# Kernel tuning notes

Hardware: AMD Instinct MI355X
Metric: run time of the kernel (lower is better)

## Reference

```python
import jax, jax.numpy as jnp
import numpy as np
import math

N_QUBITS = 6
N_LAYERS = 3
OUT_DIM = 8
B = 131072
F = 24


def _gate_rx(a):
    # RX(a) = [[cos(a/2), -i sin(a/2)], [-i sin(a/2), cos(a/2)]]; a: scalar or [B]
    c = jnp.cos(a / 2).astype(jnp.complex64)
    s = (-1j * jnp.sin(a / 2)).astype(jnp.complex64)
    return jnp.stack([jnp.stack([c, s], -1), jnp.stack([s, c], -1)], -2)


def _gate_ry(a):
    c = jnp.cos(a / 2).astype(jnp.complex64)
    s = jnp.sin(a / 2).astype(jnp.complex64)
    return jnp.stack([jnp.stack([c, -s], -1), jnp.stack([s, c], -1)], -2)


def _gate_rz(a):
    # RZ(a) = diag(e^{-ia/2}, e^{ia/2})
    e = jnp.exp(-0.5j * a.astype(jnp.complex64))
    z = jnp.zeros_like(e)
    return jnp.stack([jnp.stack([e, z], -1), jnp.stack([z, jnp.conj(e)], -1)], -2)


def _apply_1q(state, gate, q, batched):
    # state: [B] + [2]*N_QUBITS ; gate: [2,2] or [B,2,2]
    s = jnp.moveaxis(state, 1 + q, 1)
    if batched:
        out = jnp.einsum('bij,bj...->bi...', gate, s)
    else:
        out = jnp.einsum('ij,bj...->bi...', gate, s)
    return jnp.moveaxis(out, 1, 1 + q)


def _apply_cnot(state, c, t):
    # flip target where control bit == 1
    cax = 1 + c
    s0 = jnp.take(state, 0, axis=cax)
    s1 = jnp.take(state, 1, axis=cax)
    tax = 1 + t if t < c else t  # control axis removed
    s1 = jnp.flip(s1, axis=tax)
    return jnp.stack([s0, s1], axis=cax)


def _circuit(x, theta):
    Bn = x.shape[0]
    # pooling branch of forward: chunks of size ceil(F/n_qubits)=4, mean each
    x_packed = x.reshape(Bn, N_QUBITS, F // N_QUBITS).mean(-1)
    angles = jnp.clip(x_packed, -6.0, 6.0) / 6.0 * math.pi  # [B, n_qubits]

    state = jnp.zeros((Bn,) + (2,) * N_QUBITS, dtype=jnp.complex64)
    state = state.at[(slice(None),) + (0,) * N_QUBITS].set(1.0)

    # angle encoding: RX(a_q), RZ(0.5*a_q) per qubit (batched gates)
    for q in range(N_QUBITS):
        state = _apply_1q(state, _gate_rx(angles[:, q]), q, batched=True)
        state = _apply_1q(state, _gate_rz(0.5 * angles[:, q]), q, batched=True)

    for l in range(N_LAYERS):
        for q in range(N_QUBITS - 1):
            state = _apply_cnot(state, q, q + 1)
        state = _apply_cnot(state, N_QUBITS - 1, 0)
        for q in range(N_QUBITS):
            state = _apply_1q(state, _gate_rx(theta[l, q, 0]), q, batched=False)
            state = _apply_1q(state, _gate_ry(theta[l, q, 1]), q, batched=False)
            state = _apply_1q(state, _gate_rz(theta[l, q, 2]), q, batched=False)

    probs = jnp.abs(state) ** 2  # real
    meas = []
    for k in range(OUT_DIM):
        q = k % N_QUBITS
        if k % 2 == 0:  # PauliZ
            pq = jnp.sum(probs, axis=tuple(a for a in range(1, N_QUBITS + 1) if a != 1 + q))
            meas.append(pq[:, 0] - pq[:, 1])
        else:  # PauliX: Re <psi| X_q |psi>
            flipped = jnp.flip(state, axis=1 + q)
            meas.append(jnp.real(jnp.sum(jnp.conj(state) * flipped, axis=tuple(range(1, N_QUBITS + 1)))))
    return jnp.stack(meas, axis=1).astype(jnp.float32)  # [B, out_dim]


def setup_inputs() -> dict:
    key = jax.random.key(0)
    k1, k2 = jax.random.split(key)
    x = jax.random.normal(k1, (B, F), dtype=jnp.float32)
    theta = jax.random.normal(k2, (N_LAYERS, N_QUBITS, 3), dtype=jnp.float32) * 0.1
    return {"x": x, "theta": theta}


def reference(x, theta):
    return _circuit(x, theta)
```

## Files before the change

### kernel.cpp

```cpp
#include <hip/hip_runtime.h>
#include <math.h>


struct cf { float r, i; };

__device__ __forceinline__ cf cmul(cf a, cf b) {
    return { fmaf(a.r, b.r, -a.i * b.i), fmaf(a.r, b.i, a.i * b.r) };
}
__device__ __forceinline__ cf cmac(cf acc, cf g, cf v) {
    acc.r = fmaf(g.r, v.r, fmaf(-g.i, v.i, acc.r));
    acc.i = fmaf(g.r, v.i, fmaf(g.i, v.r, acc.i));
    return acc;
}

template<int M>
__device__ __forceinline__ void apply1q(cf* st, cf g00, cf g01, cf g10, cf g11) {
#pragma unroll
    for (int i = 0; i < 64; ++i) {
        if (i & M) continue;
        cf a = st[i], b = st[i + M];
        cf na = cmul(g00, a); na = cmac(na, g01, b);
        cf nb = cmul(g10, a); nb = cmac(nb, g11, b);
        st[i] = na; st[i + M] = nb;
    }
}

template<int MC, int MT>
__device__ __forceinline__ void cnot(cf* st) {
#pragma unroll
    for (int i = 0; i < 64; ++i) {
        if ((i & MC) && !(i & MT)) {
            cf tmp = st[i]; st[i] = st[i + MT]; st[i + MT] = tmp;
        }
    }
}

__global__ __launch_bounds__(256, 2) void qsim_kernel(
    const float* __restrict__ x, const float* __restrict__ theta,
    float* __restrict__ out) {
    __shared__ float gs[18 * 8];
    const int t = threadIdx.x;
    if (t < 18) {
        const float* th = theta + t * 3;
        float sx, cx, sy, cy, sz, cz;
        __sincosf(0.5f * th[0], &sx, &cx);
        __sincosf(0.5f * th[1], &sy, &cy);
        __sincosf(0.5f * th[2], &sz, &cz);
        cf m00 = {  cy * cx,  sy * sx };
        cf m01 = { -sy * cx, -cy * sx };
        cf m10 = {  sy * cx, -cy * sx };
        cf m11 = {  cy * cx, -sy * sx };
        cf e0 = { cz, -sz }, e1 = { cz, sz };
        cf g00 = cmul(e0, m00), g01 = cmul(e0, m01);
        cf g10 = cmul(e1, m10), g11 = cmul(e1, m11);
        float* o = gs + t * 8;
        o[0] = g00.r; o[1] = g00.i; o[2] = g01.r; o[3] = g01.i;
        o[4] = g10.r; o[5] = g10.i; o[6] = g11.r; o[7] = g11.i;
    }
    __syncthreads();

    const int b = blockIdx.x * 256 + t;

    const float4* xv = reinterpret_cast<const float4*>(x + (size_t)b * 24);
    cf v0[6], v1[6];
#pragma unroll
    for (int q = 0; q < 6; ++q) {
        float4 xq = xv[q];
        float m = (xq.x + xq.y + xq.z + xq.w) * 0.25f;
        m = fminf(fmaxf(m, -6.0f), 6.0f);
        float a = m * 0.52359877559829887308f;
        float s2, c2, s4, c4;
        __sincosf(0.50f * a, &s2, &c2);
        __sincosf(0.25f * a, &s4, &c4);
        v0[q] = { c4 * c2, -s4 * c2 };
        v1[q] = { s4 * s2, -c4 * s2 };
    }

    cf st[64];
    st[0] = v0[0]; st[32] = v1[0];
#pragma unroll
    for (int q = 1; q < 6; ++q) {
        const int m = 32 >> q;
#pragma unroll
        for (int i = 0; i < 64; i += 2 * m) {
            st[i + m] = cmul(st[i], v1[q]);
            st[i]     = cmul(st[i], v0[q]);
        }
    }

#pragma unroll
    for (int l = 0; l < 3; ++l) {
        cnot<32, 16>(st);
        cnot<16,  8>(st);
        cnot< 8,  4>(st);
        cnot< 4,  2>(st);
        cnot< 2,  1>(st);
        cnot< 1, 32>(st);
        const float* g = gs + l * 48;
#define G4(o) cf{g[(o)+0], g[(o)+1]}, cf{g[(o)+2], g[(o)+3]}, \
              cf{g[(o)+4], g[(o)+5]}, cf{g[(o)+6], g[(o)+7]}
        apply1q<32>(st, G4(0));
        apply1q<16>(st, G4(8));
        apply1q< 8>(st, G4(16));
        apply1q< 4>(st, G4(24));
        apply1q< 2>(st, G4(32));
        apply1q< 1>(st, G4(40));
#undef G4
    }

    float s[8] = {0, 0, 0, 0, 0, 0, 0, 0};
#pragma unroll
    for (int i = 0; i < 64; ++i) {
        float p = fmaf(st[i].r, st[i].r, st[i].i * st[i].i);
        const int gi = (((i >> 5) & 1) << 2) | (((i >> 3) & 1) << 1) | ((i >> 1) & 1);
        s[gi] += p;
    }
    float z0 = (s[0] + s[1] + s[2] + s[3]) - (s[4] + s[5] + s[6] + s[7]);
    float z2 = (s[0] + s[1] + s[4] + s[5]) - (s[2] + s[3] + s[6] + s[7]);
    float z4 = (s[0] + s[2] + s[4] + s[6]) - (s[1] + s[3] + s[5] + s[7]);

    float x1 = 0.0f, x3 = 0.0f, x5 = 0.0f;
#pragma unroll
    for (int i = 0; i < 64; ++i) {
        if (!(i & 16)) x1 = fmaf(st[i].r, st[i + 16].r, fmaf(st[i].i, st[i + 16].i, x1));
        if (!(i &  4)) x3 = fmaf(st[i].r, st[i +  4].r, fmaf(st[i].i, st[i +  4].i, x3));
        if (!(i &  1)) x5 = fmaf(st[i].r, st[i +  1].r, fmaf(st[i].i, st[i +  1].i, x5));
    }
    x1 *= 2.0f; x3 *= 2.0f; x5 *= 2.0f;

    float4* ov = reinterpret_cast<float4*>(out + (size_t)b * 8);
    ov[0] = make_float4(z0, x1, z2, x3);
    ov[1] = make_float4(z4, x5, z0, x1);
}

extern "C" void kernel_launch(void* const* d_in, const int* in_sizes, int n_in,
                              void* d_out, int out_size, void* d_ws, size_t ws_size,
                              hipStream_t stream) {
    const float* x     = (const float*)d_in[0];
    const float* theta = (const float*)d_in[1];
    float* out = (float*)d_out;
    const int B = in_sizes[0] / 24;
    qsim_kernel<<<dim3(B / 256), dim3(256), 0, stream>>>(x, theta, out);
}
```

Measured before the change: 88.73 us.

## Split each sample's 64-amplitude state across two lanes using DPP exchange

Each batch sample now runs on two adjacent threads. Each thread holds 32 amplitudes, split on the top qubit. Gates and CNOTs that touch qubit 0 use DPP quad-permute lane swaps, and the final reductions combine the two lanes' partial sums the same way. This halves the per-thread register footprint, raises launch_bounds occupancy to 4, and doubles the grid. In exchange it adds cross-lane moves, select logic and redundant per-pair x loads and sincos, and it turns off unrolling of the layer loop.

```diff
diff --git a/kernel.cpp b/kernel.cpp
--- a/kernel.cpp
+++ b/kernel.cpp
@@ -13,29 +13,34 @@
     return acc;
 }
 
+__device__ __forceinline__ float xpair(float v) {
+    return __int_as_float(__builtin_amdgcn_mov_dpp(__float_as_int(v), 0xB1, 0xF, 0xF, true));
+}
+__device__ __forceinline__ cf xpair(cf v) { return { xpair(v.r), xpair(v.i) }; }
+
 template<int M>
 __device__ __forceinline__ void apply1q(cf* st, cf g00, cf g01, cf g10, cf g11) {
 #pragma unroll
-    for (int i = 0; i < 64; ++i) {
-        if (i & M) continue;
-        cf a = st[i], b = st[i + M];
+    for (int j = 0; j < 32; ++j) {
+        if (j & M) continue;
+        cf a = st[j], b = st[j + M];
         cf na = cmul(g00, a); na = cmac(na, g01, b);
         cf nb = cmul(g10, a); nb = cmac(nb, g11, b);
-        st[i] = na; st[i + M] = nb;
+        st[j] = na; st[j + M] = nb;
     }
 }
 
 template<int MC, int MT>
 __device__ __forceinline__ void cnot(cf* st) {
 #pragma unroll
-    for (int i = 0; i < 64; ++i) {
-        if ((i & MC) && !(i & MT)) {
-            cf tmp = st[i]; st[i] = st[i + MT]; st[i + MT] = tmp;
+    for (int j = 0; j < 32; ++j) {
+        if ((j & MC) && !(j & MT)) {
+            cf tmp = st[j]; st[j] = st[j + MT]; st[j + MT] = tmp;
         }
     }
 }
 
-__global__ __launch_bounds__(256, 2) void qsim_kernel(
+__global__ __launch_bounds__(256, 4) void qsim_kernel(
     const float* __restrict__ x, const float* __restrict__ theta,
     float* __restrict__ out) {
     __shared__ float gs[18 * 8];
@@ -59,47 +64,70 @@
     }
     __syncthreads();
 
-    const int b = blockIdx.x * 256 + t;
+    const int tg = blockIdx.x * 256 + t;
+    const int b  = tg >> 1;
+    const bool pb = (tg & 1) != 0;
 
     const float4* xv = reinterpret_cast<const float4*>(x + (size_t)b * 24);
-    cf v0[6], v1[6];
+    float4 xq[6];
+#pragma unroll
+    for (int q = 0; q < 6; ++q) xq[q] = xv[q];
+
+    cf st[32];
 #pragma unroll
     for (int q = 0; q < 6; ++q) {
-        float4 xq = xv[q];
-        float m = (xq.x + xq.y + xq.z + xq.w) * 0.25f;
+        float4 v = xq[q];
+        float m = (v.x + v.y + v.z + v.w) * 0.25f;
         m = fminf(fmaxf(m, -6.0f), 6.0f);
         float a = m * 0.52359877559829887308f;
         float s2, c2, s4, c4;
         __sincosf(0.50f * a, &s2, &c2);
         __sincosf(0.25f * a, &s4, &c4);
-        v0[q] = { c4 * c2, -s4 * c2 };
-        v1[q] = { s4 * s2, -c4 * s2 };
-    }
-
-    cf st[64];
-    st[0] = v0[0]; st[32] = v1[0];
+        cf v0 = { c4 * c2, -s4 * c2 };
+        cf v1 = { s4 * s2, -c4 * s2 };
+        if (q == 0) {
+            st[0] = pb ? v1 : v0;
+        } else {
+            const int mq = 32 >> q;
 #pragma unroll
-    for (int q = 1; q < 6; ++q) {
-        const int m = 32 >> q;
-#pragma unroll
-        for (int i = 0; i < 64; i += 2 * m) {
-            st[i + m] = cmul(st[i], v1[q]);
-            st[i]     = cmul(st[i], v0[q]);
+            for (int i = 0; i < 32; i += 2 * mq) {
+                st[i + mq] = cmul(st[i], v1);
+                st[i]      = cmul(st[i], v0);
+            }
         }
     }
 
+#pragma unroll 1
+    for (int l = 0; l < 3; ++l) {
 #pragma unroll
-    for (int l = 0; l < 3; ++l) {
-        cnot<32, 16>(st);
-        cnot<16,  8>(st);
-        cnot< 8,  4>(st);
-        cnot< 4,  2>(st);
-        cnot< 2,  1>(st);
-        cnot< 1, 32>(st);
+        for (int j = 0; j < 16; ++j) {
+            cf lo = st[j], hi = st[j + 16];
+            st[j]      = pb ? hi : lo;
+            st[j + 16] = pb ? lo : hi;
+        }
+        cnot<16, 8>(st);
+        cnot< 8, 4>(st);
+        cnot< 4, 2>(st);
+        cnot< 2, 1>(st);
+#pragma unroll
+        for (int j = 1; j < 32; j += 2) st[j] = xpair(st[j]);
+
         const float* g = gs + l * 48;
+
+        {
+            cf q00 = { g[0], g[1] }, q01 = { g[2], g[3] };
+            cf q10 = { g[4], g[5] }, q11 = { g[6], g[7] };
+            cf gm = pb ? q11 : q00;
+            cf go = pb ? q10 : q01;
+#pragma unroll
+            for (int j = 0; j < 32; ++j) {
+                cf other = xpair(st[j]);
+                cf nv = cmul(gm, st[j]);
+                st[j] = cmac(nv, go, other);
+            }
+        }
 #define G4(o) cf{g[(o)+0], g[(o)+1]}, cf{g[(o)+2], g[(o)+3]}, \
               cf{g[(o)+4], g[(o)+5]}, cf{g[(o)+6], g[(o)+7]}
-        apply1q<32>(st, G4(0));
         apply1q<16>(st, G4(8));
         apply1q< 8>(st, G4(16));
         apply1q< 4>(st, G4(24));
@@ -108,29 +136,36 @@
 #undef G4
     }
 
-    float s[8] = {0, 0, 0, 0, 0, 0, 0, 0};
+    float s[4] = { 0, 0, 0, 0 };
 #pragma unroll
-    for (int i = 0; i < 64; ++i) {
-        float p = fmaf(st[i].r, st[i].r, st[i].i * st[i].i);
-        const int gi = (((i >> 5) & 1) << 2) | (((i >> 3) & 1) << 1) | ((i >> 1) & 1);
-        s[gi] += p;
+    for (int j = 0; j < 32; ++j) {
+        float pj = fmaf(st[j].r, st[j].r, st[j].i * st[j].i);
+        const int gi = (((j >> 3) & 1) << 1) | ((j >> 1) & 1);
+        s[gi] += pj;
     }
-    float z0 = (s[0] + s[1] + s[2] + s[3]) - (s[4] + s[5] + s[6] + s[7]);
-    float z2 = (s[0] + s[1] + s[4] + s[5]) - (s[2] + s[3] + s[6] + s[7]);
-    float z4 = (s[0] + s[2] + s[4] + s[6]) - (s[1] + s[3] + s[5] + s[7]);
+    float tot = (s[0] + s[1]) + (s[2] + s[3]);
+    float z0 = pb ? -tot : tot;
+    float z2 = (s[0] + s[1]) - (s[2] + s[3]);
+    float z4 = (s[0] + s[2]) - (s[1] + s[3]);
 
-    float x1 = 0.0f, x3 = 0.0f, x5 = 0.0f;
+    float x1 = 0.f, x3 = 0.f, x5 = 0.f;
 #pragma unroll
-    for (int i = 0; i < 64; ++i) {
-        if (!(i & 16)) x1 = fmaf(st[i].r, st[i + 16].r, fmaf(st[i].i, st[i + 16].i, x1));
-        if (!(i &  4)) x3 = fmaf(st[i].r, st[i +  4].r, fmaf(st[i].i, st[i +  4].i, x3));
-        if (!(i &  1)) x5 = fmaf(st[i].r, st[i +  1].r, fmaf(st[i].i, st[i +  1].i, x5));
+    for (int j = 0; j < 32; ++j) {
+        if (!(j & 16)) x1 = fmaf(st[j].r, st[j + 16].r, fmaf(st[j].i, st[j + 16].i, x1));
+        if (!(j &  4)) x3 = fmaf(st[j].r, st[j +  4].r, fmaf(st[j].i, st[j +  4].i, x3));
+        if (!(j &  1)) x5 = fmaf(st[j].r, st[j +  1].r, fmaf(st[j].i, st[j +  1].i, x5));
     }
-    x1 *= 2.0f; x3 *= 2.0f; x5 *= 2.0f;
 
+    z0 += xpair(z0); z2 += xpair(z2); z4 += xpair(z4);
+    x1 += xpair(x1); x3 += xpair(x3); x5 += xpair(x5);
+    x1 *= 2.f; x3 *= 2.f; x5 *= 2.f;
+
+    float oa = pb ? z4 : z0;
+    float ob = pb ? x5 : x1;
+    float oc = pb ? z0 : z2;
+    float od = pb ? x1 : x3;
     float4* ov = reinterpret_cast<float4*>(out + (size_t)b * 8);
-    ov[0] = make_float4(z0, x1, z2, x3);
-    ov[1] = make_float4(z4, x5, z0, x1);
+    ov[pb ? 1 : 0] = make_float4(oa, ob, oc, od);
 }
 
 extern "C" void kernel_launch(void* const* d_in, const int* in_sizes, int n_in,
@@ -140,5 +175,5 @@
     const float* theta = (const float*)d_in[1];
     float* out = (float*)d_out;
     const int B = in_sizes[0] / 24;
-    qsim_kernel<<<dim3(B / 256), dim3(256), 0, stream>>>(x, theta, out);
+    qsim_kernel<<<dim3((B * 2) / 256), dim3(256), 0, stream>>>(x, theta, out);
 }
```

New measurement: 99.66 us. 12.3% more time.

## Use packed FP32 inline asm for complex gate math and reductions

Applied to the files above, without the earlier changes.

Replaces scalar complex multiply and multiply-accumulate with v_pk_mul_f32/v_pk_fma_f32 inline assembly on float2, aiming to halve the VALU instruction count of the state-vector gate updates and the measurement reductions. Gate coefficients are now stored in LDS as float2. The layer loop is no longer unrolled and the min-blocks launch bound is dropped, which changes register allocation and adds per-layer LDS gate loads. The inline asm limits what the compiler can schedule across it.

```diff
diff --git a/kernel.cpp b/kernel.cpp
--- a/kernel.cpp
+++ b/kernel.cpp
@@ -2,43 +2,62 @@
 #include <math.h>
 
 
-struct cf { float r, i; };
-
-__device__ __forceinline__ cf cmul(cf a, cf b) {
-    return { fmaf(a.r, b.r, -a.i * b.i), fmaf(a.r, b.i, a.i * b.r) };
+__device__ __forceinline__ float2 pk_cmul(float2 g, float2 a) {
+    float2 t;
+    asm("v_pk_mul_f32 %0, %1, %2 op_sel:[0,0] op_sel_hi:[0,1]"
+        : "=v"(t) : "v"(g), "v"(a));
+    asm("v_pk_fma_f32 %0, %1, %2, %0 op_sel:[1,1,0] op_sel_hi:[1,0,1] neg_lo:[1,0,0]"
+        : "+v"(t) : "v"(g), "v"(a));
+    return t;
 }
-__device__ __forceinline__ cf cmac(cf acc, cf g, cf v) {
-    acc.r = fmaf(g.r, v.r, fmaf(-g.i, v.i, acc.r));
-    acc.i = fmaf(g.r, v.i, fmaf(g.i, v.r, acc.i));
+__device__ __forceinline__ float2 pk_cmac(float2 acc, float2 g, float2 a) {
+    asm("v_pk_fma_f32 %0, %1, %2, %0 op_sel:[0,0,0] op_sel_hi:[0,1,1]"
+        : "+v"(acc) : "v"(g), "v"(a));
+    asm("v_pk_fma_f32 %0, %1, %2, %0 op_sel:[1,1,0] op_sel_hi:[1,0,1] neg_lo:[1,0,0]"
+        : "+v"(acc) : "v"(g), "v"(a));
+    return acc;
+}
+__device__ __forceinline__ float2 pk_sqacc(float2 acc, float2 a) {
+    asm("v_pk_fma_f32 %0, %1, %1, %0" : "+v"(acc) : "v"(a));
+    return acc;
+}
+__device__ __forceinline__ float2 pk_macv(float2 acc, float2 a, float2 b) {
+    asm("v_pk_fma_f32 %0, %1, %2, %0" : "+v"(acc) : "v"(a), "v"(b));
     return acc;
 }
 
 template<int M>
-__device__ __forceinline__ void apply1q(cf* st, cf g00, cf g01, cf g10, cf g11) {
+__device__ __forceinline__ void apply1q(float2* st, float2 g00, float2 g01,
+                                        float2 g10, float2 g11) {
 #pragma unroll
     for (int i = 0; i < 64; ++i) {
         if (i & M) continue;
-        cf a = st[i], b = st[i + M];
-        cf na = cmul(g00, a); na = cmac(na, g01, b);
-        cf nb = cmul(g10, a); nb = cmac(nb, g11, b);
+        float2 a = st[i], b = st[i + M];
+        float2 na = pk_cmul(g00, a); na = pk_cmac(na, g01, b);
+        float2 nb = pk_cmul(g10, a); nb = pk_cmac(nb, g11, b);
         st[i] = na; st[i + M] = nb;
     }
 }
 
 template<int MC, int MT>
-__device__ __forceinline__ void cnot(cf* st) {
+__device__ __forceinline__ void cnot(float2* st) {
 #pragma unroll
     for (int i = 0; i < 64; ++i) {
         if ((i & MC) && !(i & MT)) {
-            cf tmp = st[i]; st[i] = st[i + MT]; st[i + MT] = tmp;
+            float2 tmp = st[i]; st[i] = st[i + MT]; st[i + MT] = tmp;
         }
     }
 }
 
-__global__ __launch_bounds__(256, 2) void qsim_kernel(
+struct cf { float r, i; };
+__device__ __forceinline__ cf scmul(cf a, cf b) {
+    return { fmaf(a.r, b.r, -a.i * b.i), fmaf(a.r, b.i, a.i * b.r) };
+}
+
+__global__ __launch_bounds__(256) void qsim_kernel(
     const float* __restrict__ x, const float* __restrict__ theta,
     float* __restrict__ out) {
-    __shared__ float gs[18 * 8];
+    __shared__ float2 gs[18 * 4];
     const int t = threadIdx.x;
     if (t < 18) {
         const float* th = theta + t * 3;
@@ -51,18 +70,20 @@
         cf m10 = {  sy * cx, -cy * sx };
         cf m11 = {  cy * cx, -sy * sx };
         cf e0 = { cz, -sz }, e1 = { cz, sz };
-        cf g00 = cmul(e0, m00), g01 = cmul(e0, m01);
-        cf g10 = cmul(e1, m10), g11 = cmul(e1, m11);
-        float* o = gs + t * 8;
-        o[0] = g00.r; o[1] = g00.i; o[2] = g01.r; o[3] = g01.i;
-        o[4] = g10.r; o[5] = g10.i; o[6] = g11.r; o[7] = g11.i;
+        cf g00 = scmul(e0, m00), g01 = scmul(e0, m01);
+        cf g10 = scmul(e1, m10), g11 = scmul(e1, m11);
+        float2* o = gs + t * 4;
+        o[0] = make_float2(g00.r, g00.i);
+        o[1] = make_float2(g01.r, g01.i);
+        o[2] = make_float2(g10.r, g10.i);
+        o[3] = make_float2(g11.r, g11.i);
     }
     __syncthreads();
 
     const int b = blockIdx.x * 256 + t;
 
     const float4* xv = reinterpret_cast<const float4*>(x + (size_t)b * 24);
-    cf v0[6], v1[6];
+    float2 v0[6], v1[6];
 #pragma unroll
     for (int q = 0; q < 6; ++q) {
         float4 xq = xv[q];
@@ -72,23 +93,23 @@
         float s2, c2, s4, c4;
         __sincosf(0.50f * a, &s2, &c2);
         __sincosf(0.25f * a, &s4, &c4);
-        v0[q] = { c4 * c2, -s4 * c2 };
-        v1[q] = { s4 * s2, -c4 * s2 };
+        v0[q] = make_float2(c4 * c2, -s4 * c2);
+        v1[q] = make_float2(s4 * s2, -c4 * s2);
     }
 
-    cf st[64];
+    float2 st[64];
     st[0] = v0[0]; st[32] = v1[0];
 #pragma unroll
     for (int q = 1; q < 6; ++q) {
         const int m = 32 >> q;
 #pragma unroll
         for (int i = 0; i < 64; i += 2 * m) {
-            st[i + m] = cmul(st[i], v1[q]);
-            st[i]     = cmul(st[i], v0[q]);
+            st[i + m] = pk_cmul(st[i], v1[q]);
+            st[i]     = pk_cmul(st[i], v0[q]);
         }
     }
 
-#pragma unroll
+#pragma unroll 1
     for (int l = 0; l < 3; ++l) {
         cnot<32, 16>(st);
         cnot<16,  8>(st);
@@ -96,37 +117,40 @@
         cnot< 4,  2>(st);
         cnot< 2,  1>(st);
         cnot< 1, 32>(st);
-        const float* g = gs + l * 48;
-#define G4(o) cf{g[(o)+0], g[(o)+1]}, cf{g[(o)+2], g[(o)+3]}, \
-              cf{g[(o)+4], g[(o)+5]}, cf{g[(o)+6], g[(o)+7]}
-        apply1q<32>(st, G4(0));
-        apply1q<16>(st, G4(8));
-        apply1q< 8>(st, G4(16));
-        apply1q< 4>(st, G4(24));
-        apply1q< 2>(st, G4(32));
-        apply1q< 1>(st, G4(40));
-#undef G4
+        const float2* g = gs + l * 24;
+        apply1q<32>(st, g[ 0], g[ 1], g[ 2], g[ 3]);
+        apply1q<16>(st, g[ 4], g[ 5], g[ 6], g[ 7]);
+        apply1q< 8>(st, g[ 8], g[ 9], g[10], g[11]);
+        apply1q< 4>(st, g[12], g[13], g[14], g[15]);
+        apply1q< 2>(st, g[16], g[17], g[18], g[19]);
+        apply1q< 1>(st, g[20], g[21], g[22], g[23]);
     }
 
-    float s[8] = {0, 0, 0, 0, 0, 0, 0, 0};
+    float2 ps[8];
+#pragma unroll
+    for (int k = 0; k < 8; ++k) ps[k] = make_float2(0.f, 0.f);
 #pragma unroll
     for (int i = 0; i < 64; ++i) {
-        float p = fmaf(st[i].r, st[i].r, st[i].i * st[i].i);
         const int gi = (((i >> 5) & 1) << 2) | (((i >> 3) & 1) << 1) | ((i >> 1) & 1);
-        s[gi] += p;
+        ps[gi] = pk_sqacc(ps[gi], st[i]);
     }
+    float s[8];
+#pragma unroll
+    for (int k = 0; k < 8; ++k) s[k] = ps[k].x + ps[k].y;
     float z0 = (s[0] + s[1] + s[2] + s[3]) - (s[4] + s[5] + s[6] + s[7]);
     float z2 = (s[0] + s[1] + s[4] + s[5]) - (s[2] + s[3] + s[6] + s[7]);
     float z4 = (s[0] + s[2] + s[4] + s[6]) - (s[1] + s[3] + s[5] + s[7]);
 
-    float x1 = 0.0f, x3 = 0.0f, x5 = 0.0f;
+    float2 xa = make_float2(0.f, 0.f), xb = xa, xc = xa;
 #pragma unroll
     for (int i = 0; i < 64; ++i) {
-        if (!(i & 16)) x1 = fmaf(st[i].r, st[i + 16].r, fmaf(st[i].i, st[i + 16].i, x1));
-        if (!(i &  4)) x3 = fmaf(st[i].r, st[i +  4].r, fmaf(st[i].i, st[i +  4].i, x3));
-        if (!(i &  1)) x5 = fmaf(st[i].r, st[i +  1].r, fmaf(st[i].i, st[i +  1].i, x5));
+        if (!(i & 16)) xa = pk_macv(xa, st[i], st[i + 16]);
+        if (!(i &  4)) xb = pk_macv(xb, st[i], st[i +  4]);
+        if (!(i &  1)) xc = pk_macv(xc, st[i], st[i +  1]);
     }
-    x1 *= 2.0f; x3 *= 2.0f; x5 *= 2.0f;
+    float x1 = 2.f * (xa.x + xa.y);
+    float x3 = 2.f * (xb.x + xb.y);
+    float x5 = 2.f * (xc.x + xc.y);
 
     float4* ov = reinterpret_cast<float4*>(out + (size_t)b * 8);
     ov[0] = make_float4(z0, x1, z2, x3);
```

After: 83.45 us. -5.9%, faster.
